# Optimization experiments

Hardware: AMD Instinct MI355X
Metric: run time of the kernel (lower is better)

Reference implementation:

```python
import jax, jax.numpy as jnp
import numpy as np

S, P, H, E = 32, 32, 128, 64        # scenes, peds/scene, h_dim, embedding_dim
B1, B2 = 512, 1024                  # mlp_pre_pool hidden, bottleneck_dim
M1 = 1024                           # decoder mlp hidden
N = S * P
T = 12                              # seq_len (decode horizon)
BN_INV = 1.0 / np.sqrt(1.0 + 1e-5)  # eval-mode BatchNorm, running mean=0 var=1


def setup_inputs() -> dict:
    key = jax.random.key(0)
    ks = jax.random.split(key, 32)
    rn = lambda k, sh, s=0.05: jax.random.normal(k, sh, dtype=jnp.float32) * s
    inp = {
        'last_pos': rn(ks[0], (N, 2), 1.0),
        'last_pos_rel': rn(ks[1], (N, 2), 1.0),
        'h0': rn(ks[2], (N, H), 0.1),
        'c0': rn(ks[3], (N, H), 0.1),
        'seq_start_end': jnp.stack([jnp.arange(S) * P, (jnp.arange(S) + 1) * P], 1).astype(jnp.int32),
        # decoder spatial embedding Linear(2, E)
        'emb_W': rn(ks[4], (E, 2)), 'emb_b': rn(ks[5], (E,)),
        # LSTM (torch gate order i,f,g,o)
        'lstm_Wih': rn(ks[6], (4 * H, E)), 'lstm_Whh': rn(ks[7], (4 * H, H)),
        'lstm_bih': rn(ks[8], (4 * H,)), 'lstm_bhh': rn(ks[9], (4 * H,)),
        # hidden2pos Linear(H, 2)
        'pos_W': rn(ks[10], (2, H)), 'pos_b': rn(ks[11], (2,)),
        # pool_net spatial embedding Linear(2, E)
        'sp_W': rn(ks[12], (E, 2)), 'sp_b': rn(ks[13], (E,)),
        # mlp_pre_pool: Linear(E+H, 512)+BN+ReLU, Linear(512, 1024)+BN+ReLU
        'pp1_W': rn(ks[14], (B1, E + H)), 'pp1_b': rn(ks[15], (B1,)),
        'pp1_g': 1.0 + rn(ks[16], (B1,)), 'pp1_be': rn(ks[17], (B1,)),
        'pp2_W': rn(ks[18], (B2, B1)), 'pp2_b': rn(ks[19], (B2,)),
        'pp2_g': 1.0 + rn(ks[20], (B2,)), 'pp2_be': rn(ks[21], (B2,)),
        # decoder mlp: Linear(H+1024, 1024)+BN+ReLU, Linear(1024, H)+BN+ReLU
        'm1_W': rn(ks[22], (M1, H + B2)), 'm1_b': rn(ks[23], (M1,)),
        'm1_g': 1.0 + rn(ks[24], (M1,)), 'm1_be': rn(ks[25], (M1,)),
        'm2_W': rn(ks[26], (H, M1)), 'm2_b': rn(ks[27], (H,)),
        'm2_g': 1.0 + rn(ks[28], (H,)), 'm2_be': rn(ks[29], (H,)),
    }
    return inp


def _bn(x, g, b):
    return x * BN_INV * g + b


def reference(last_pos, last_pos_rel, h0, c0, seq_start_end,
              emb_W, emb_b, lstm_Wih, lstm_Whh, lstm_bih, lstm_bhh,
              pos_W, pos_b, sp_W, sp_b,
              pp1_W, pp1_b, pp1_g, pp1_be, pp2_W, pp2_b, pp2_g, pp2_be,
              m1_W, m1_b, m1_g, m1_be, m2_W, m2_b, m2_g, m2_be):
    # seq_start_end encodes uniform scenes of size P; pooling is done per scene.
    def step(carry, _):
        h, c, lp, din = carry  # h,c:[N,H]  lp:[N,2]  din:[N,E]
        gates = din @ lstm_Wih.T + lstm_bih + h @ lstm_Whh.T + lstm_bhh
        i, f, g_, o = jnp.split(gates, 4, axis=-1)
        c2 = jax.nn.sigmoid(f) * c + jax.nn.sigmoid(i) * jnp.tanh(g_)
        h2 = jax.nn.sigmoid(o) * jnp.tanh(c2)
        rel_pos = h2 @ pos_W.T + pos_b          # [N,2]
        curr = rel_pos + lp                     # [N,2]
        # ---- PoolHiddenNet: per-scene all-pairs gather -> MLP -> max ----
        ps = curr.reshape(S, P, 2)
        rel = ps[:, None, :, :] - ps[:, :, None, :]   # [s,i,j] = pos_j - pos_i
        rel = rel / jnp.maximum(jnp.linalg.norm(rel, axis=-1, keepdims=True), 1e-12)
        emb = rel @ sp_W.T + sp_b                      # [S,P,P,E]
        hj = jnp.broadcast_to(h2.reshape(S, 1, P, H), (S, P, P, H))
        x = jnp.concatenate([emb, hj], -1)             # [S,P,P,E+H]
        x = jax.nn.relu(_bn(x @ pp1_W.T + pp1_b, pp1_g, pp1_be))
        x = jax.nn.relu(_bn(x @ pp2_W.T + pp2_b, pp2_g, pp2_be))
        pool = x.max(axis=2).reshape(N, B2)            # max over neighbours j
        # ---- hidden refinement MLP ----
        dh = jnp.concatenate([h2, pool], 1)
        dh = jax.nn.relu(_bn(dh @ m1_W.T + m1_b, m1_g, m1_be))
        dh = jax.nn.relu(_bn(dh @ m2_W.T + m2_b, m2_g, m2_be))
        din2 = rel_pos @ emb_W.T + emb_b
        return (dh, c2, curr, din2), rel_pos

    din0 = last_pos_rel @ emb_W.T + emb_b
    _, preds = jax.lax.scan(step, (h0, c0, last_pos, din0), None, length=T)
    return preds  # [T, N, 2] predicted relative displacements
```

## Files before the change

### kernel.cpp

```cpp
#include <hip/hip_runtime.h>
#include <hip/hip_bf16.h>
#include <math.h>

#define DEVFN __device__ __forceinline__

constexpr float BN_INV = 0.99999500003749971f;

DEVFN float sigm(float x) { return 1.0f / (1.0f + expf(-x)); }

DEVFN unsigned short f2bf(float f) {
    __hip_bfloat16 b = __float2bfloat16(f);
    return *reinterpret_cast<unsigned short*>(&b);
}
DEVFN float bf2f(unsigned short u) {
    unsigned int x = ((unsigned int)u) << 16;
    return *reinterpret_cast<float*>(&x);
}
DEVFN void splitf(float v, unsigned short& h, unsigned short& l) {
    h = f2bf(v);
    l = f2bf(v - bf2f(h));
}
DEVFN unsigned int pack2(unsigned short a, unsigned short b) {
    return (unsigned int)a | ((unsigned int)b << 16);
}

typedef __attribute__((ext_vector_type(8))) short short8;
typedef __attribute__((ext_vector_type(4))) float f32x4;

#define ASYNC_COPY16(gsrc, ldst)                                                            \
    __builtin_amdgcn_global_load_lds((const __attribute__((address_space(1))) unsigned int*)(gsrc), \
                                     (__attribute__((address_space(3))) unsigned int*)(ldst), 16, 0, 0)


__global__ void pre_lstm(const float* __restrict__ Wih, const float* __restrict__ Whh,
                         const float* __restrict__ bih, const float* __restrict__ bhh,
                         float* __restrict__ WgT, float* __restrict__ bg) {
    int idx = blockIdx.x * blockDim.x + threadIdx.x;
    int k = idx >> 9, t = idx & 511;
    WgT[idx] = (k < 64) ? Wih[t * 64 + k] : Whh[t * 128 + (k - 64)];
    if (idx < 512) bg[idx] = bih[idx] + bhh[idx];
}

__global__ void pre_wh1(const float* __restrict__ pp1W, const float* __restrict__ pp1g,
                        float* __restrict__ Wh1T) {
    int idx = blockIdx.x * blockDim.x + threadIdx.x;
    int h = idx >> 9, k = idx & 511;
    Wh1T[idx] = pp1W[k * 192 + 64 + h] * (BN_INV * pp1g[k]);
}

__global__ void pre_mp(const float* __restrict__ spW, const float* __restrict__ spb,
                       const float* __restrict__ pp1W, const float* __restrict__ pp1b,
                       const float* __restrict__ pp1g, const float* __restrict__ pp1be,
                       float* __restrict__ Mp, float* __restrict__ c1) {
    int k = blockIdx.x * blockDim.x + threadIdx.x;
    float m0 = 0.f, m1 = 0.f, c0 = 0.f;
    for (int e = 0; e < 64; e++) {
        float w = pp1W[k * 192 + e];
        m0 += spW[e * 2] * w; m1 += spW[e * 2 + 1] * w; c0 += spb[e] * w;
    }
    float s = BN_INV * pp1g[k];
    Mp[k] = m0 * s; Mp[512 + k] = m1 * s;
    c1[k] = (c0 + pp1b[k]) * s + pp1be[k];
}

__global__ void pre_w2bf(const float* __restrict__ W, const float* __restrict__ b,
                         const float* __restrict__ g, const float* __restrict__ be,
                         unsigned short* __restrict__ Wbf, float* __restrict__ cv, int swz) {
    int idx = blockIdx.x * blockDim.x + threadIdx.x;
    int ko = idx >> 9, k = idx & 511;
    float s = BN_INV * g[ko];
    int outk = swz ? ((k & ~63) | ((((k >> 3) & 7) ^ (ko & 7)) << 3) | (k & 7)) : k;
    Wbf[(ko << 9) + outk] = f2bf(W[idx] * s);
    if (idx < 1024) cv[idx] = b[idx] * s + be[idx];
}

__global__ void pre_w1split(const float* __restrict__ W, const float* __restrict__ b,
                            const float* __restrict__ g, const float* __restrict__ be,
                            unsigned short* __restrict__ Wh, unsigned short* __restrict__ Wl,
                            float* __restrict__ cv) {
    int idx = blockIdx.x * blockDim.x + threadIdx.x;
    int ko = idx / 1152;
    float s = BN_INV * g[ko];
    unsigned short h, l;
    splitf(W[idx] * s, h, l);
    Wh[idx] = h; Wl[idx] = l;
    if (idx < 1024) {
        float s2 = BN_INV * g[idx];
        cv[idx] = b[idx] * s2 + be[idx];
    }
}

__global__ void pre_w2split(const float* __restrict__ W, const float* __restrict__ b,
                            const float* __restrict__ g, const float* __restrict__ be,
                            unsigned short* __restrict__ Wh, unsigned short* __restrict__ Wl,
                            float* __restrict__ cv) {
    int idx = blockIdx.x * blockDim.x + threadIdx.x;
    int ko = idx >> 10;
    float s = BN_INV * g[ko];
    unsigned short h, l;
    splitf(W[idx] * s, h, l);
    Wh[idx] = h; Wl[idx] = l;
    if (idx < 128) {
        float s2 = BN_INV * g[idx];
        cv[idx] = b[idx] * s2 + be[idx];
    }
}

__global__ void pre_init(const float* __restrict__ lp, const float* __restrict__ lpr,
                         const float* __restrict__ h0, const float* __restrict__ c0,
                         const float* __restrict__ embW, const float* __restrict__ embb,
                         float* __restrict__ h_st, float* __restrict__ c_st,
                         float* __restrict__ curr, float* __restrict__ din) {
    int idx = blockIdx.x * blockDim.x + threadIdx.x;
    h_st[idx] = h0[idx];
    c_st[idx] = c0[idx];
    if (idx < 1024 * 2) curr[idx] = lp[idx];
    if (idx < 1024 * 64) {
        int n = idx >> 6, e = idx & 63;
        din[idx] = fmaf(lpr[n * 2], embW[e * 2], fmaf(lpr[n * 2 + 1], embW[e * 2 + 1], embb[e]));
    }
}


__global__ __launch_bounds__(512) void k_lstm(
    const float* __restrict__ WgT, const float* __restrict__ bg,
    float* __restrict__ h_st, float* __restrict__ c_st,
    float* __restrict__ din, float* __restrict__ curr,
    unsigned short* __restrict__ h2h, unsigned short* __restrict__ h2l,
    const float* __restrict__ posW, const float* __restrict__ posb,
    const float* __restrict__ embW, const float* __restrict__ embb,
    const float* __restrict__ Wh1T, const float* __restrict__ c1,
    float* __restrict__ Hp, int doHp,
    float* __restrict__ preds) {
    int n0 = blockIdx.x << 2;
    int t = threadIdx.x;
    __shared__ float xs[4][256];
    __shared__ float gates[4][512];
    __shared__ float h2s[4][128];
    __shared__ float rp[4][2];
#pragma unroll
    for (int u = 0; u < 2; u++) {
        int lin = t + (u << 9);
        int r = lin >> 8, k = lin & 255;
        float v = 0.f;
        if (k < 64) v = din[(n0 + r) * 64 + k];
        else if (k < 192) v = h_st[(n0 + r) * 128 + (k - 64)];
        xs[r][k] = v;
    }
    __syncthreads();
    float a0 = bg[t], a1 = a0, a2 = a0, a3 = a0;
#pragma unroll 4
    for (int k = 0; k < 192; k++) {
        float w = WgT[(k << 9) + t];
        a0 = fmaf(xs[0][k], w, a0);
        a1 = fmaf(xs[1][k], w, a1);
        a2 = fmaf(xs[2][k], w, a2);
        a3 = fmaf(xs[3][k], w, a3);
    }
    gates[0][t] = a0; gates[1][t] = a1; gates[2][t] = a2; gates[3][t] = a3;
    __syncthreads();
    {
        int r = t >> 7, hx = t & 127;
        float ig = sigm(gates[r][hx]);
        float fg = sigm(gates[r][128 + hx]);
        float gg = tanhf(gates[r][256 + hx]);
        float og = sigm(gates[r][384 + hx]);
        float c2 = fmaf(fg, c_st[(n0 + r) * 128 + hx], ig * gg);
        float h2 = og * tanhf(c2);
        c_st[(n0 + r) * 128 + hx] = c2;
        unsigned short sh, sl;
        splitf(h2, sh, sl);
        h2h[(n0 + r) * 128 + hx] = sh;
        h2l[(n0 + r) * 128 + hx] = sl;
        h2s[r][hx] = h2;
    }
    __syncthreads();
    int wv = t >> 6, l = t & 63;
    if (wv < 4) {
        float p0 = fmaf(h2s[wv][l], posW[l], h2s[wv][l + 64] * posW[l + 64]);
        float p1 = fmaf(h2s[wv][l], posW[128 + l], h2s[wv][l + 64] * posW[192 + l]);
#pragma unroll
        for (int off = 32; off > 0; off >>= 1) {
            p0 += __shfl_down(p0, off, 64);
            p1 += __shfl_down(p1, off, 64);
        }
        if (l == 0) { rp[wv][0] = p0 + posb[0]; rp[wv][1] = p1 + posb[1]; }
    }
    __syncthreads();
    if (t < 256) {
        int r = t >> 6, e = t & 63;
        float r0 = rp[r][0], r1 = rp[r][1];
        din[(n0 + r) * 64 + e] = fmaf(r0, embW[e * 2], fmaf(r1, embW[e * 2 + 1], embb[e]));
        if (e == 0) {
            preds[(n0 + r) * 2] = r0; preds[(n0 + r) * 2 + 1] = r1;
            curr[(n0 + r) * 2] += r0; curr[(n0 + r) * 2 + 1] += r1;
        }
    }
    if (doHp) {
        float cc = c1[t];
        float q0 = cc, q1 = cc, q2 = cc, q3 = cc;
#pragma unroll 4
        for (int h = 0; h < 128; h++) {
            float w = Wh1T[(h << 9) + t];
            q0 = fmaf(h2s[0][h], w, q0);
            q1 = fmaf(h2s[1][h], w, q1);
            q2 = fmaf(h2s[2][h], w, q2);
            q3 = fmaf(h2s[3][h], w, q3);
        }
        Hp[((n0 + 0) << 9) + t] = q0;
        Hp[((n0 + 1) << 9) + t] = q1;
        Hp[((n0 + 2) << 9) + t] = q2;
        Hp[((n0 + 3) << 9) + t] = q3;
    }
}

__global__ __launch_bounds__(256) void k_x1(
    const float* __restrict__ Hp, const float* __restrict__ Mp,
    const float* __restrict__ curr, unsigned short* __restrict__ x1g) {
    int bid = blockIdx.x;
    int c = bid & 7, q = bid >> 3;
    int i = q & 31, g = q >> 5;
    int s = (g << 3) + c;
    int si = (s << 5) + i;
    int t = threadIdx.x;
    __shared__ float rx[32], ry[32];
    __shared__ float m0s[512], m1s[512];
    for (int u = t; u < 512; u += 256) { m0s[u] = Mp[u]; m1s[u] = Mp[512 + u]; }
    if (t < 32) {
        int jg = (s << 5) + t;
        float dx = curr[jg * 2] - curr[si * 2];
        float dy = curr[jg * 2 + 1] - curr[si * 2 + 1];
        float den = fmaxf(sqrtf(dx * dx + dy * dy), 1e-12f);
        rx[t] = dx / den; ry[t] = dy / den;
    }
    __syncthreads();
    int j = t >> 3, c8 = t & 7;
    float rxv = rx[j], ryv = ry[j];
    const float* hp = Hp + (((s << 5) + j) << 9);
    unsigned short* op = x1g + ((size_t)((si << 5) + j) << 9);
    int swz = (c8 ^ (j & 7)) << 3;
#pragma unroll
    for (int kt = 0; kt < 512; kt += 64) {
        int k = kt + (c8 << 3);
        float4 ha = *(const float4*)(hp + k);
        float4 hb = *(const float4*)(hp + k + 4);
        uint4 o;
        o.x = pack2(f2bf(fmaxf(fmaf(rxv, m0s[k + 0], fmaf(ryv, m1s[k + 0], ha.x)), 0.f)),
                    f2bf(fmaxf(fmaf(rxv, m0s[k + 1], fmaf(ryv, m1s[k + 1], ha.y)), 0.f)));
        o.y = pack2(f2bf(fmaxf(fmaf(rxv, m0s[k + 2], fmaf(ryv, m1s[k + 2], ha.z)), 0.f)),
                    f2bf(fmaxf(fmaf(rxv, m0s[k + 3], fmaf(ryv, m1s[k + 3], ha.w)), 0.f)));
        o.z = pack2(f2bf(fmaxf(fmaf(rxv, m0s[k + 4], fmaf(ryv, m1s[k + 4], hb.x)), 0.f)),
                    f2bf(fmaxf(fmaf(rxv, m0s[k + 5], fmaf(ryv, m1s[k + 5], hb.y)), 0.f)));
        o.w = pack2(f2bf(fmaxf(fmaf(rxv, m0s[k + 6], fmaf(ryv, m1s[k + 6], hb.z)), 0.f)),
                    f2bf(fmaxf(fmaf(rxv, m0s[k + 7], fmaf(ryv, m1s[k + 7], hb.w)), 0.f)));
        *(uint4*)(op + kt + swz) = o;
    }
}

__global__ __launch_bounds__(256) void k_pool_g(
    const unsigned short* __restrict__ x1g, const unsigned short* __restrict__ W2bf,
    const float* __restrict__ c2v,
    unsigned short* __restrict__ poolh, unsigned short* __restrict__ pooll) {
    int bid = blockIdx.x;
    int c = bid & 7, q = bid >> 3;
    int inner = q & 63, g = q >> 6;
    int s = (g << 3) + c;
    int rb = inner >> 3;
    int koBase = (inner & 7) << 7;
    int t = threadIdx.x;
    int lane = t & 63, wv = t >> 6;
    int quad = lane >> 4, l15 = lane & 15;
    int qrow = (wv >> 1) << 6, qcol = (wv & 1) << 6;
    __shared__ unsigned short As[128 * 64];
    __shared__ unsigned short Bs[128 * 64];
    f32x4 acc[4][4];
#pragma unroll
    for (int a = 0; a < 4; a++)
#pragma unroll
        for (int b = 0; b < 4; b++) acc[a][b] = (f32x4){0.f, 0.f, 0.f, 0.f};

    int rowG0 = (s << 10) + (rb << 7);
    int rlane = lane >> 3;
    int clane = (lane & 7) << 3;

    for (int kt = 0; kt < 512; kt += 64) {
#pragma unroll
        for (int u = 0; u < 4; u++) {
            int r = (wv << 5) + (u << 3);
            ASYNC_COPY16(x1g + (size_t)(rowG0 + r + rlane) * 512 + kt + clane, &As[r << 6]);
            ASYNC_COPY16(W2bf + (size_t)(koBase + r + rlane) * 512 + kt + clane, &Bs[r << 6]);
        }
        __syncthreads();
#pragma unroll
        for (int kt2 = 0; kt2 < 2; kt2++) {
            short8 aF[4], bF[4];
#pragma unroll
            for (int a = 0; a < 4; a++) {
                int r = qrow + (a << 4) + l15;
                int pos = ((kt2 << 2) + quad) ^ (r & 7);
                aF[a] = *(const short8*)(&As[(r << 6) + (pos << 3)]);
            }
#pragma unroll
            for (int b = 0; b < 4; b++) {
                int r = qcol + (b << 4) + l15;
                int pos = ((kt2 << 2) + quad) ^ (r & 7);
                bF[b] = *(const short8*)(&Bs[(r << 6) + (pos << 3)]);
            }
#pragma unroll
            for (int a = 0; a < 4; a++)
#pragma unroll
                for (int b = 0; b < 4; b++)
                    acc[a][b] = __builtin_amdgcn_mfma_f32_16x16x32_bf16(aF[a], bF[b], acc[a][b], 0, 0, 0);
        }
        __syncthreads();
    }

    float mx0[4], mx1[4];
#pragma unroll
    for (int b = 0; b < 4; b++) {
        float m = acc[0][b].x;
#pragma unroll
        for (int a = 0; a < 2; a++) {
            m = fmaxf(m, acc[a][b].x); m = fmaxf(m, acc[a][b].y);
            m = fmaxf(m, acc[a][b].z); m = fmaxf(m, acc[a][b].w);
        }
        m = fmaxf(m, __shfl_xor(m, 16));
        m = fmaxf(m, __shfl_xor(m, 32));
        mx0[b] = m;
        float n = acc[2][b].x;
#pragma unroll
        for (int a = 2; a < 4; a++) {
            n = fmaxf(n, acc[a][b].x); n = fmaxf(n, acc[a][b].y);
            n = fmaxf(n, acc[a][b].z); n = fmaxf(n, acc[a][b].w);
        }
        n = fmaxf(n, __shfl_xor(n, 16));
        n = fmaxf(n, __shfl_xor(n, 32));
        mx1[b] = n;
    }
    float v0 = (quad == 0) ? mx0[0] : (quad == 1) ? mx0[1] : (quad == 2) ? mx0[2] : mx0[3];
    float v1 = (quad == 0) ? mx1[0] : (quad == 1) ? mx1[1] : (quad == 2) ? mx1[2] : mx1[3];
    int col = koBase + qcol + (quad << 4) + l15;
    int i0 = (rb << 2) + ((wv >> 1) << 1);
    int si0 = (s << 5) + i0;
    float bias = c2v[col];
    float w0 = fmaxf(v0 + bias, 0.f);
    float w1 = fmaxf(v1 + bias, 0.f);
    unsigned short h0, l0, h1, l1;
    splitf(w0, h0, l0); splitf(w1, h1, l1);
    poolh[si0 * 1024 + col] = h0; pooll[si0 * 1024 + col] = l0;
    poolh[(si0 + 1) * 1024 + col] = h1; pooll[(si0 + 1) * 1024 + col] = l1;
}

__global__ __launch_bounds__(256) void k_pool_mfma(
    const float* __restrict__ Hp, const float* __restrict__ Mp,
    const unsigned short* __restrict__ W2bf,
    const float* __restrict__ c2v, const float* __restrict__ curr,
    unsigned short* __restrict__ poolh, unsigned short* __restrict__ pooll) {
    int s = blockIdx.z;
    int rb = blockIdx.y;
    int koBase = blockIdx.x << 7;
    int t = threadIdx.x;
    int lane = t & 63, wv = t >> 6;
    int quad = lane >> 4, l15 = lane & 15;
    int qrow = (wv >> 1) << 6;
    int qcol = (wv & 1) << 6;

    __shared__ unsigned short As[128 * 40];
    __shared__ unsigned short Bs[128 * 40];
    __shared__ float rx[128], ry[128];

    if (t < 128) {
        int iL = t >> 5, j = t & 31;
        int ig = (s << 5) + (rb << 2) + iL;
        int jg = (s << 5) + j;
        float dx = curr[jg * 2] - curr[ig * 2];
        float dy = curr[jg * 2 + 1] - curr[ig * 2 + 1];
        float den = fmaxf(sqrtf(dx * dx + dy * dy), 1e-12f);
        rx[t] = dx / den; ry[t] = dy / den;
    }
    __syncthreads();

    f32x4 acc[4][4];
#pragma unroll
    for (int a = 0; a < 4; a++)
#pragma unroll
        for (int b = 0; b < 4; b++) acc[a][b] = (f32x4){0.f, 0.f, 0.f, 0.f};

    int r0 = t >> 3, c4 = (t & 7) << 2;
    int bn = t >> 1, bk = (t & 1) << 4;

    for (int kt = 0; kt < 512; kt += 32) {
#pragma unroll
        for (int p = 0; p < 4; p++) {
            int rr = r0 + (p << 5);
            int j = rr & 31;
            int kg = kt + c4;
            float4 hv = *(const float4*)(Hp + (((s << 5) + j) << 9) + kg);
            float4 m0 = *(const float4*)(Mp + kg);
            float4 m1 = *(const float4*)(Mp + 512 + kg);
            float rxv = rx[rr], ryv = ry[rr];
            float v0 = fmaxf(fmaf(rxv, m0.x, fmaf(ryv, m1.x, hv.x)), 0.f);
            float v1 = fmaxf(fmaf(rxv, m0.y, fmaf(ryv, m1.y, hv.y)), 0.f);
            float v2 = fmaxf(fmaf(rxv, m0.z, fmaf(ryv, m1.z, hv.z)), 0.f);
            float v3 = fmaxf(fmaf(rxv, m0.w, fmaf(ryv, m1.w, hv.w)), 0.f);
            unsigned int u0 = pack2(f2bf(v0), f2bf(v1));
            unsigned int u1 = pack2(f2bf(v2), f2bf(v3));
            *(uint2*)(&As[rr * 40 + c4]) = make_uint2(u0, u1);
        }
        {
            const unsigned short* src = W2bf + (((koBase + bn) << 9) + kt + bk);
            uint4 w0 = *(const uint4*)src;
            uint4 w1 = *(const uint4*)(src + 8);
            *(uint4*)(&Bs[bn * 40 + bk]) = w0;
            *(uint4*)(&Bs[bn * 40 + bk + 8]) = w1;
        }
        __syncthreads();
        short8 bF[4];
#pragma unroll
        for (int b = 0; b < 4; b++)
            bF[b] = *(const short8*)(&Bs[(qcol + (b << 4) + l15) * 40 + (quad << 3)]);
#pragma unroll
        for (int a = 0; a < 4; a++) {
            short8 aF = *(const short8*)(&As[(qrow + (a << 4) + l15) * 40 + (quad << 3)]);
#pragma unroll
            for (int b = 0; b < 4; b++)
                acc[a][b] = __builtin_amdgcn_mfma_f32_16x16x32_bf16(aF, bF[b], acc[a][b], 0, 0, 0);
        }
        __syncthreads();
    }

    float mx0[4], mx1[4];
#pragma unroll
    for (int b = 0; b < 4; b++) {
        float m = acc[0][b].x;
#pragma unroll
        for (int a = 0; a < 2; a++) {
            m = fmaxf(m, acc[a][b].x); m = fmaxf(m, acc[a][b].y);
            m = fmaxf(m, acc[a][b].z); m = fmaxf(m, acc[a][b].w);
        }
        m = fmaxf(m, __shfl_xor(m, 16));
        m = fmaxf(m, __shfl_xor(m, 32));
        mx0[b] = m;
        float n = acc[2][b].x;
#pragma unroll
        for (int a = 2; a < 4; a++) {
            n = fmaxf(n, acc[a][b].x); n = fmaxf(n, acc[a][b].y);
            n = fmaxf(n, acc[a][b].z); n = fmaxf(n, acc[a][b].w);
        }
        n = fmaxf(n, __shfl_xor(n, 16));
        n = fmaxf(n, __shfl_xor(n, 32));
        mx1[b] = n;
    }
    float v0 = (quad == 0) ? mx0[0] : (quad == 1) ? mx0[1] : (quad == 2) ? mx0[2] : mx0[3];
    float v1 = (quad == 0) ? mx1[0] : (quad == 1) ? mx1[1] : (quad == 2) ? mx1[2] : mx1[3];
    int col = koBase + qcol + (quad << 4) + l15;
    int i0 = (rb << 2) + ((wv >> 1) << 1);
    int si0 = (s << 5) + i0;
    float bias = c2v[col];
    float w0 = fmaxf(v0 + bias, 0.f);
    float w1 = fmaxf(v1 + bias, 0.f);
    unsigned short h0, l0, h1, l1;
    splitf(w0, h0, l0); splitf(w1, h1, l1);
    poolh[si0 * 1024 + col] = h0; pooll[si0 * 1024 + col] = l0;
    poolh[(si0 + 1) * 1024 + col] = h1; pooll[(si0 + 1) * 1024 + col] = l1;
}

__global__ __launch_bounds__(256) void k_m1_mfma(
    const unsigned short* __restrict__ h2h, const unsigned short* __restrict__ h2l,
    const unsigned short* __restrict__ poolh, const unsigned short* __restrict__ pooll,
    const unsigned short* __restrict__ M1h, const unsigned short* __restrict__ M1l,
    const float* __restrict__ cm1,
    unsigned short* __restrict__ dh1h, unsigned short* __restrict__ dh1l) {
    int rowBase = blockIdx.y << 6;
    int koBase = blockIdx.x << 6;
    int t = threadIdx.x;
    int lane = t & 63, wv = t >> 6;
    int quad = lane >> 4, l15 = lane & 15;
    int qrow = (wv >> 1) << 5, qcol = (wv & 1) << 5;
    __shared__ unsigned short Ah[64 * 40], Al[64 * 40], Bh[64 * 40], Bl[64 * 40];
    f32x4 acc[2][2];
#pragma unroll
    for (int a = 0; a < 2; a++)
#pragma unroll
        for (int b = 0; b < 2; b++) acc[a][b] = (f32x4){0.f, 0.f, 0.f, 0.f};

    int ar = t >> 2, ak = (t & 3) << 3;

    for (int kt = 0; kt < 1152; kt += 32) {
        {
            const unsigned short* sH;
            const unsigned short* sL;
            int off;
            if (kt < 128) {
                off = (rowBase + ar) * 128 + kt + ak;
                sH = h2h; sL = h2l;
            } else {
                off = (rowBase + ar) * 1024 + (kt - 128) + ak;
                sH = poolh; sL = pooll;
            }
            *(uint4*)&Ah[ar * 40 + ak] = *(const uint4*)(sH + off);
            *(uint4*)&Al[ar * 40 + ak] = *(const uint4*)(sL + off);
        }
        {
            int boff = (koBase + ar) * 1152 + kt + ak;
            *(uint4*)&Bh[ar * 40 + ak] = *(const uint4*)(M1h + boff);
            *(uint4*)&Bl[ar * 40 + ak] = *(const uint4*)(M1l + boff);
        }
        __syncthreads();
        short8 bH[2], bL[2];
#pragma unroll
        for (int b = 0; b < 2; b++) {
            int boff = (qcol + (b << 4) + l15) * 40 + (quad << 3);
            bH[b] = *(const short8*)(&Bh[boff]);
            bL[b] = *(const short8*)(&Bl[boff]);
        }
#pragma unroll
        for (int a = 0; a < 2; a++) {
            int aoff = (qrow + (a << 4) + l15) * 40 + (quad << 3);
            short8 aH = *(const short8*)(&Ah[aoff]);
            short8 aL = *(const short8*)(&Al[aoff]);
#pragma unroll
            for (int b = 0; b < 2; b++) {
                acc[a][b] = __builtin_amdgcn_mfma_f32_16x16x32_bf16(aH, bH[b], acc[a][b], 0, 0, 0);
                acc[a][b] = __builtin_amdgcn_mfma_f32_16x16x32_bf16(aH, bL[b], acc[a][b], 0, 0, 0);
                acc[a][b] = __builtin_amdgcn_mfma_f32_16x16x32_bf16(aL, bH[b], acc[a][b], 0, 0, 0);
            }
        }
        __syncthreads();
    }
#pragma unroll
    for (int b = 0; b < 2; b++) {
        int col = koBase + qcol + (b << 4) + l15;
        float bias = cm1[col];
#pragma unroll
        for (int a = 0; a < 2; a++) {
#pragma unroll
            for (int rg = 0; rg < 4; rg++) {
                int row = rowBase + qrow + (a << 4) + (quad << 2) + rg;
                float v = fmaxf(acc[a][b][rg] + bias, 0.f);
                unsigned short sh, sl;
                splitf(v, sh, sl);
                dh1h[row * 1024 + col] = sh;
                dh1l[row * 1024 + col] = sl;
            }
        }
    }
}

__global__ __launch_bounds__(256) void k_m2_mfma(
    const unsigned short* __restrict__ dh1h, const unsigned short* __restrict__ dh1l,
    const unsigned short* __restrict__ M2h, const unsigned short* __restrict__ M2l,
    const float* __restrict__ cm2, float* __restrict__ h_st) {
    int rowBase = blockIdx.x << 6;
    int t = threadIdx.x;
    int lane = t & 63, wv = t >> 6;
    int quad = lane >> 4, l15 = lane & 15;
    int qrow = (wv >> 1) << 5;
    int qcol = (wv & 1) << 6;
    __shared__ unsigned short Ah[64 * 40], Al[64 * 40], Bh[128 * 40], Bl[128 * 40];
    f32x4 acc[2][4];
#pragma unroll
    for (int a = 0; a < 2; a++)
#pragma unroll
        for (int b = 0; b < 4; b++) acc[a][b] = (f32x4){0.f, 0.f, 0.f, 0.f};

    int ar = t >> 2, ak = (t & 3) << 3;
    int br = t >> 1, bk = (t & 1) << 4;

    for (int kt = 0; kt < 1024; kt += 32) {
        {
            int off = (rowBase + ar) * 1024 + kt + ak;
            *(uint4*)&Ah[ar * 40 + ak] = *(const uint4*)(dh1h + off);
            *(uint4*)&Al[ar * 40 + ak] = *(const uint4*)(dh1l + off);
        }
        {
            int off = br * 1024 + kt + bk;
            *(uint4*)&Bh[br * 40 + bk] = *(const uint4*)(M2h + off);
            *(uint4*)&Bh[br * 40 + bk + 8] = *(const uint4*)(M2h + off + 8);
            *(uint4*)&Bl[br * 40 + bk] = *(const uint4*)(M2l + off);
            *(uint4*)&Bl[br * 40 + bk + 8] = *(const uint4*)(M2l + off + 8);
        }
        __syncthreads();
#pragma unroll
        for (int a = 0; a < 2; a++) {
            int aoff = (qrow + (a << 4) + l15) * 40 + (quad << 3);
            short8 aH = *(const short8*)(&Ah[aoff]);
            short8 aL = *(const short8*)(&Al[aoff]);
#pragma unroll
            for (int b = 0; b < 4; b++) {
                int boff = (qcol + (b << 4) + l15) * 40 + (quad << 3);
                short8 bH = *(const short8*)(&Bh[boff]);
                short8 bL = *(const short8*)(&Bl[boff]);
                acc[a][b] = __builtin_amdgcn_mfma_f32_16x16x32_bf16(aH, bH, acc[a][b], 0, 0, 0);
                acc[a][b] = __builtin_amdgcn_mfma_f32_16x16x32_bf16(aH, bL, acc[a][b], 0, 0, 0);
                acc[a][b] = __builtin_amdgcn_mfma_f32_16x16x32_bf16(aL, bH, acc[a][b], 0, 0, 0);
            }
        }
        __syncthreads();
    }
#pragma unroll
    for (int b = 0; b < 4; b++) {
        int col = qcol + (b << 4) + l15;
        float bias = cm2[col];
#pragma unroll
        for (int a = 0; a < 2; a++) {
#pragma unroll
            for (int rg = 0; rg < 4; rg++) {
                int row = rowBase + qrow + (a << 4) + (quad << 2) + rg;
                h_st[row * 128 + col] = fmaxf(acc[a][b][rg] + bias, 0.f);
            }
        }
    }
}


extern "C" void kernel_launch(void* const* d_in, const int* in_sizes, int n_in,
                              void* d_out, int out_size, void* d_ws, size_t ws_size,
                              hipStream_t stream) {
    const float* last_pos     = (const float*)d_in[0];
    const float* last_pos_rel = (const float*)d_in[1];
    const float* h0   = (const float*)d_in[2];
    const float* c0   = (const float*)d_in[3];
    const float* emb_W = (const float*)d_in[5];
    const float* emb_b = (const float*)d_in[6];
    const float* lstm_Wih = (const float*)d_in[7];
    const float* lstm_Whh = (const float*)d_in[8];
    const float* lstm_bih = (const float*)d_in[9];
    const float* lstm_bhh = (const float*)d_in[10];
    const float* pos_W = (const float*)d_in[11];
    const float* pos_b = (const float*)d_in[12];
    const float* sp_W  = (const float*)d_in[13];
    const float* sp_b  = (const float*)d_in[14];
    const float* pp1_W = (const float*)d_in[15];
    const float* pp1_b = (const float*)d_in[16];
    const float* pp1_g = (const float*)d_in[17];
    const float* pp1_be= (const float*)d_in[18];
    const float* pp2_W = (const float*)d_in[19];
    const float* pp2_b = (const float*)d_in[20];
    const float* pp2_g = (const float*)d_in[21];
    const float* pp2_be= (const float*)d_in[22];
    const float* m1_W  = (const float*)d_in[23];
    const float* m1_b  = (const float*)d_in[24];
    const float* m1_g  = (const float*)d_in[25];
    const float* m1_be = (const float*)d_in[26];
    const float* m2_W  = (const float*)d_in[27];
    const float* m2_b  = (const float*)d_in[28];
    const float* m2_g  = (const float*)d_in[29];
    const float* m2_be = (const float*)d_in[30];
    float* out = (float*)d_out;

    float* p = (float*)d_ws;
    float* WgT  = p; p += 192 * 512;
    float* bg   = p; p += 512;
    float* Wh1T = p; p += 128 * 512;
    float* Mp   = p; p += 2 * 512;
    float* c1   = p; p += 512;
    unsigned short* W2bf = (unsigned short*)p; p += 512 * 1024 / 2;
    float* c2v  = p; p += 1024;
    unsigned short* M1h = (unsigned short*)p; p += 1024 * 1152 / 2;
    unsigned short* M1l = (unsigned short*)p; p += 1024 * 1152 / 2;
    float* cm1  = p; p += 1024;
    unsigned short* M2h = (unsigned short*)p; p += 128 * 1024 / 2;
    unsigned short* M2l = (unsigned short*)p; p += 128 * 1024 / 2;
    float* cm2  = p; p += 128;
    float* h_st = p; p += 1024 * 128;
    float* c_st = p; p += 1024 * 128;
    unsigned short* h2h = (unsigned short*)p; p += 1024 * 128 / 2;
    unsigned short* h2l = (unsigned short*)p; p += 1024 * 128 / 2;
    float* curr = p; p += 1024 * 2;
    float* din  = p; p += 1024 * 64;
    float* Hp   = p; p += 1024 * 512;
    unsigned short* poolh = (unsigned short*)p; p += 1024 * 1024 / 2;
    unsigned short* pooll = (unsigned short*)p; p += 1024 * 1024 / 2;
    unsigned short* dh1h = (unsigned short*)p; p += 1024 * 1024 / 2;
    unsigned short* dh1l = (unsigned short*)p; p += 1024 * 1024 / 2;
    unsigned short* x1g = (unsigned short*)p;
    size_t need = (size_t)((char*)(x1g + (size_t)32768 * 512) - (char*)d_ws);
    int big = (ws_size >= need) ? 1 : 0;

    pre_lstm<<<384, 256, 0, stream>>>(lstm_Wih, lstm_Whh, lstm_bih, lstm_bhh, WgT, bg);
    pre_wh1<<<256, 256, 0, stream>>>(pp1_W, pp1_g, Wh1T);
    pre_mp<<<2, 256, 0, stream>>>(sp_W, sp_b, pp1_W, pp1_b, pp1_g, pp1_be, Mp, c1);
    pre_w2bf<<<2048, 256, 0, stream>>>(pp2_W, pp2_b, pp2_g, pp2_be, W2bf, c2v, big);
    pre_w1split<<<4608, 256, 0, stream>>>(m1_W, m1_b, m1_g, m1_be, M1h, M1l, cm1);
    pre_w2split<<<512, 256, 0, stream>>>(m2_W, m2_b, m2_g, m2_be, M2h, M2l, cm2);
    pre_init<<<512, 256, 0, stream>>>(last_pos, last_pos_rel, h0, c0, emb_W, emb_b,
                                      h_st, c_st, curr, din);

    for (int t = 0; t < 12; t++) {
        k_lstm<<<256, 512, 0, stream>>>(WgT, bg, h_st, c_st, din, curr, h2h, h2l,
                                        pos_W, pos_b, emb_W, emb_b,
                                        Wh1T, c1, Hp, (t < 11) ? 1 : 0, out + t * 2048);
        if (t == 11) break;
        if (big) {
            k_x1<<<1024, 256, 0, stream>>>(Hp, Mp, curr, x1g);
            k_pool_g<<<2048, 256, 0, stream>>>(x1g, W2bf, c2v, poolh, pooll);
        } else {
            k_pool_mfma<<<dim3(8, 8, 32), 256, 0, stream>>>(Hp, Mp, W2bf, c2v, curr,
                                                            poolh, pooll);
        }
        k_m1_mfma<<<dim3(16, 16), 256, 0, stream>>>(h2h, h2l, poolh, pooll,
                                                    M1h, M1l, cm1, dh1h, dh1l);
        k_m2_mfma<<<16, 256, 0, stream>>>(dh1h, dh1l, M2h, M2l, cm2, h_st);
    }
}
```

Baseline: 1.622 ms.

## Enlarge pool GEMM tile to 256x256 with 1024-thread blocks

The pooling GEMM kernel now uses 1024-thread blocks covering a 256x256 output tile, with 16 waves each computing a 64x64 sub-tile, instead of 256-thread blocks with 128x128 tiles. Grid size drops from 2048 to 512. Each loaded A/B tile is reused across more output and fewer redundant global loads are issued, and LDS fragment addresses are precomputed outside the k loop. The cost is 64KB of shared memory per block and lower occupancy, so there is less latency hiding, and the launch-bounds hint of 4 blocks per CU may not be achievable.

```diff
diff --git a/kernel.cpp b/kernel.cpp
--- a/kernel.cpp
+++ b/kernel.cpp
@@ -257,55 +257,61 @@
     }
 }
 
-__global__ __launch_bounds__(256) void k_pool_g(
+__global__ __launch_bounds__(1024, 4) void k_pool_g(
     const unsigned short* __restrict__ x1g, const unsigned short* __restrict__ W2bf,
     const float* __restrict__ c2v,
     unsigned short* __restrict__ poolh, unsigned short* __restrict__ pooll) {
     int bid = blockIdx.x;
     int c = bid & 7, q = bid >> 3;
-    int inner = q & 63, g = q >> 6;
+    int inner = q & 15, g = q >> 4;
     int s = (g << 3) + c;
-    int rb = inner >> 3;
-    int koBase = (inner & 7) << 7;
+    int rb = inner >> 2;
+    int koB = (inner & 3) << 8;
     int t = threadIdx.x;
     int lane = t & 63, wv = t >> 6;
     int quad = lane >> 4, l15 = lane & 15;
-    int qrow = (wv >> 1) << 6, qcol = (wv & 1) << 6;
-    __shared__ unsigned short As[128 * 64];
-    __shared__ unsigned short Bs[128 * 64];
+    int wr = wv >> 2, wc = wv & 3;
+    int qrow = wr << 6, qcol = wc << 6;
+    __shared__ unsigned short As[256 * 64];
+    __shared__ unsigned short Bs[256 * 64];
     f32x4 acc[4][4];
 #pragma unroll
     for (int a = 0; a < 4; a++)
 #pragma unroll
         for (int b = 0; b < 4; b++) acc[a][b] = (f32x4){0.f, 0.f, 0.f, 0.f};
 
-    int rowG0 = (s << 10) + (rb << 7);
     int rlane = lane >> 3;
     int clane = (lane & 7) << 3;
+    const unsigned short* gA = x1g + (size_t)((s << 10) + (rb << 8) + (wv << 4) + rlane) * 512 + clane;
+    const unsigned short* gB = W2bf + (size_t)(koB + (wv << 4) + rlane) * 512 + clane;
+    unsigned short* lA = As + (wv << 10);
+    unsigned short* lB = Bs + (wv << 10);
+    const unsigned short* pa0 = As + ((qrow + l15) << 6) + ((quad ^ (l15 & 7)) << 3);
+    const unsigned short* pb0 = Bs + ((qcol + l15) << 6) + ((quad ^ (l15 & 7)) << 3);
+    const unsigned short* pa1 = As + ((qrow + l15) << 6) + (((4 + quad) ^ (l15 & 7)) << 3);
+    const unsigned short* pb1 = Bs + ((qcol + l15) << 6) + (((4 + quad) ^ (l15 & 7)) << 3);
 
     for (int kt = 0; kt < 512; kt += 64) {
-#pragma unroll
-        for (int u = 0; u < 4; u++) {
-            int r = (wv << 5) + (u << 3);
-            ASYNC_COPY16(x1g + (size_t)(rowG0 + r + rlane) * 512 + kt + clane, &As[r << 6]);
-            ASYNC_COPY16(W2bf + (size_t)(koBase + r + rlane) * 512 + kt + clane, &Bs[r << 6]);
-        }
+        ASYNC_COPY16(gA + kt, lA);
+        ASYNC_COPY16(gA + kt + 8 * 512, lA + (8 << 6));
+        ASYNC_COPY16(gB + kt, lB);
+        ASYNC_COPY16(gB + kt + 8 * 512, lB + (8 << 6));
         __syncthreads();
-#pragma unroll
-        for (int kt2 = 0; kt2 < 2; kt2++) {
+        {
             short8 aF[4], bF[4];
 #pragma unroll
-            for (int a = 0; a < 4; a++) {
-                int r = qrow + (a << 4) + l15;
-                int pos = ((kt2 << 2) + quad) ^ (r & 7);
-                aF[a] = *(const short8*)(&As[(r << 6) + (pos << 3)]);
-            }
-#pragma unroll
-            for (int b = 0; b < 4; b++) {
-                int r = qcol + (b << 4) + l15;
-                int pos = ((kt2 << 2) + quad) ^ (r & 7);
-                bF[b] = *(const short8*)(&Bs[(r << 6) + (pos << 3)]);
-            }
+            for (int a = 0; a < 4; a++) aF[a] = *(const short8*)(pa0 + (a << 10));
+#pragma unroll
+            for (int b = 0; b < 4; b++) bF[b] = *(const short8*)(pb0 + (b << 10));
+#pragma unroll
+            for (int a = 0; a < 4; a++)
+#pragma unroll
+                for (int b = 0; b < 4; b++)
+                    acc[a][b] = __builtin_amdgcn_mfma_f32_16x16x32_bf16(aF[a], bF[b], acc[a][b], 0, 0, 0);
+#pragma unroll
+            for (int a = 0; a < 4; a++) aF[a] = *(const short8*)(pa1 + (a << 10));
+#pragma unroll
+            for (int b = 0; b < 4; b++) bF[b] = *(const short8*)(pb1 + (b << 10));
 #pragma unroll
             for (int a = 0; a < 4; a++)
 #pragma unroll
@@ -339,8 +345,8 @@
     }
     float v0 = (quad == 0) ? mx0[0] : (quad == 1) ? mx0[1] : (quad == 2) ? mx0[2] : mx0[3];
     float v1 = (quad == 0) ? mx1[0] : (quad == 1) ? mx1[1] : (quad == 2) ? mx1[2] : mx1[3];
-    int col = koBase + qcol + (quad << 4) + l15;
-    int i0 = (rb << 2) + ((wv >> 1) << 1);
+    int col = koB + qcol + (quad << 4) + l15;
+    int i0 = (rb << 3) + (wr << 1);
     int si0 = (s << 5) + i0;
     float bias = c2v[col];
     float w0 = fmaxf(v0 + bias, 0.f);
@@ -694,7 +700,7 @@
         if (t == 11) break;
         if (big) {
             k_x1<<<1024, 256, 0, stream>>>(Hp, Mp, curr, x1g);
-            k_pool_g<<<2048, 256, 0, stream>>>(x1g, W2bf, c2v, poolh, pooll);
+            k_pool_g<<<512, 1024, 0, stream>>>(x1g, W2bf, c2v, poolh, pooll);
         } else {
             k_pool_mfma<<<dim3(8, 8, 32), 256, 0, stream>>>(Hp, Mp, W2bf, c2v, curr,
                                                             poolh, pooll);
```

After: 1.517 ms. 6.5% less time.
